# Performance work log

Measured on AMD Instinct MI355X. Metric: run time of the kernel, lower is better.

Reference implementation:

```python
import jax, jax.numpy as jnp
import numpy as np

_EPS = 1e-5

def _ln(x, g, b):
    m = jnp.mean(x, axis=-1, keepdims=True)
    v = jnp.var(x, axis=-1, keepdims=True)
    return (x - m) * jax.lax.rsqrt(v + _EPS) * g + b

def setup_inputs() -> dict:
    key = jax.random.key(0)
    ks = jax.random.split(key, 12)
    B, S, D = 8, 2048, 1024
    H = 2 * D          # hidden_dim = 2*n_embd
    A = H // 16        # adapt_dim = 128
    E = 8              # num_experts
    std = 1.0 / D ** 0.5
    astd = std * 0.01
    f = lambda k, shape, s: jax.random.normal(k, shape, dtype=jnp.float32) * s
    return {
        'x': f(ks[0], (B, S, D), 1.0),
        'expert_weights': f(ks[1], (B, S, E), 1.0),
        'w_up': f(ks[2], (H, D), std),
        'w_gate': f(ks[3], (H, D), std),
        'w_down': f(ks[4], (D, H), std),
        'w_pre': f(ks[5], (A, D), astd),
        'w_post': f(ks[6], (A, H), astd),
        'an_g': jnp.ones((A,), jnp.float32),
        'an_b': jnp.zeros((A,), jnp.float32),
        'w_aproj': f(ks[7], (H, A), astd),
        'w_exp': f(ks[8], (E, A, A), 0.01 / A ** 0.5),
        'eln_g': jnp.ones((E, A), jnp.float32),
        'eln_b': jnp.zeros((E, A), jnp.float32),
        'w_eproj': f(ks[9], (H, A), 0.01 / A ** 0.5),
        'w_out': f(ks[10], (D, H), 0.01 / A ** 0.5),
    }

def reference(x, expert_weights, w_up, w_gate, w_down, w_pre, w_post,
              an_g, an_b, w_aproj, w_exp, eln_g, eln_b, w_eproj, w_out):
    # ---- shared LLaDAExpert ----
    up = jnp.einsum('bsd,hd->bsh', x, w_up)
    gate = jnp.einsum('bsd,hd->bsh', x, w_gate)
    hidden = jax.nn.silu(gate) * up                      # [B,S,H]
    pre = jnp.einsum('bsd,ad->bsa', x, w_pre)            # pre_adapt(x), reused by experts
    adapt_in = _ln(pre, an_g, an_b)                      # [B,S,A]
    adapt_out = _ln(jnp.einsum('bsh,ah->bsa', hidden, w_post), an_g, an_b)
    aw = jax.nn.silu(jnp.clip(jnp.einsum('bsa,bta->bst', adapt_in, adapt_out), -5.0, 5.0))  # [B,S,S]
    adapt = jnp.einsum('bst,bta->bsa', aw, adapt_in)     # [B,S,A]
    hidden = hidden + 0.1 * jnp.einsum('bsa,ha->bsh', adapt, w_aproj)
    shared = jnp.einsum('bsh,dh->bsd', hidden, w_down)   # [B,S,D]
    combined = jnp.zeros_like(shared)
    E = w_exp.shape[0]
    for i in range(E):
        a = _ln(jnp.einsum('bsa,ca->bsc', pre, w_exp[i]), eln_g[i], eln_b[i])
        o = jnp.einsum('bsh,dh->bsd', jnp.einsum('bsc,hc->bsh', a, w_eproj), w_out)
        mask = expert_weights[:, :, i] > 0
        combined = jnp.where(mask[..., None], o, combined)
    return shared + 0.1 * combined
```

## Files before the change

kernel.cpp:

```cpp
#include <hip/hip_runtime.h>

#define TOK 16384
#define DD 1024
#define HH 2048
#define AA 128
#define EE 8
#define SS 2048
#define BB 8

typedef __attribute__((ext_vector_type(8))) short short8;
typedef __attribute__((ext_vector_type(4))) float floatx4;

__device__ __forceinline__ unsigned short f2b(float f) {
  unsigned u = __float_as_uint(f);
  u += 0x7fff + ((u >> 16) & 1);
  return (unsigned short)(u >> 16);
}
__device__ __forceinline__ float b2f(unsigned short h) {
  return __uint_as_float(((unsigned)h) << 16);
}

__device__ __forceinline__ void xcd_swizzle(int& bx, int& by) {
  const int nbx = gridDim.x, nby = gridDim.y;
  if ((nby & 7) == 0) {
    const int L = blockIdx.y * nbx + blockIdx.x;
    const int xcd = L & 7, idx = L >> 3;
    bx = idx % nbx;
    by = (xcd * (nby >> 3)) + idx / nbx;
  } else {
    bx = blockIdx.x; by = blockIdx.y;
  }
}


__device__ __forceinline__ void gload16(const short* g, short* l) {
  __builtin_amdgcn_global_load_lds((__attribute__((address_space(1))) void*)(void*)g,
                                   (__attribute__((address_space(3))) void*)l, 16, 0, 0);
}

__device__ __forceinline__ void stage_tile(const short* src, int ld, short* dst, int wave) {
#pragma unroll
  for (int i = 0; i < 4; ++i)
    gload16(src + (long)i*64*ld, dst + i*4096 + wave*512);
}

#define MFMA_BLK(MM0, NN0)                                                               \
  __builtin_amdgcn_s_setprio(1);                                                         \
  _Pragma("unroll")                                                                      \
  for (int m = 0; m < 4; ++m)                                                            \
    _Pragma("unroll")                                                                    \
    for (int n = 0; n < 2; ++n) {                                                        \
      acc[MM0+m][NN0+n] = __builtin_amdgcn_mfma_f32_16x16x32_bf16(af[MM0+m][0], bf[NN0+n][0], acc[MM0+m][NN0+n], 0, 0, 0); \
      acc[MM0+m][NN0+n] = __builtin_amdgcn_mfma_f32_16x16x32_bf16(af[MM0+m][1], bf[NN0+n][1], acc[MM0+m][NN0+n], 0, 0, 0); \
    }                                                                                    \
  __builtin_amdgcn_s_setprio(0);

__device__ __forceinline__ void ktile256(const char* Ab, const char* Bb,
                                         const char* An, const char* Bn,
                                         short* Ad, short* Bd,
                                         const short* sA, int slda,
                                         const short* sB, int sldb,
                                         bool st, bool rd, int wave,
                                         int aOff, int bOff, int slot0, int slot1,
                                         short8 (&af)[8][2], short8 (&bf)[4][2],
                                         floatx4 (*acc)[4])
{
#pragma unroll
  for (int n = 2; n < 4; ++n) {
    bf[n][0] = *(const short8*)(Bb + bOff + n*2048 + slot0);
    bf[n][1] = *(const short8*)(Bb + bOff + n*2048 + slot1);
  }
  MFMA_BLK(0, 0)
#pragma unroll
  for (int m = 4; m < 8; ++m) {
    af[m][0] = *(const short8*)(Ab + aOff + m*2048 + slot0);
    af[m][1] = *(const short8*)(Ab + aOff + m*2048 + slot1);
  }
  MFMA_BLK(0, 2)
  asm volatile("s_waitcnt lgkmcnt(0)" ::: "memory");
  __builtin_amdgcn_s_barrier();
  if (st) stage_tile(sB, sldb, Bd, wave);
  MFMA_BLK(4, 0)
  if (st) asm volatile("s_waitcnt vmcnt(4)" ::: "memory");
  else    asm volatile("s_waitcnt vmcnt(0)" ::: "memory");
  __builtin_amdgcn_s_barrier();
  if (rd) {
#pragma unroll
    for (int m = 0; m < 4; ++m) {
      af[m][0] = *(const short8*)(An + aOff + m*2048 + slot0);
      af[m][1] = *(const short8*)(An + aOff + m*2048 + slot1);
    }
#pragma unroll
    for (int n = 0; n < 2; ++n) {
      bf[n][0] = *(const short8*)(Bn + bOff + n*2048 + slot0);
      bf[n][1] = *(const short8*)(Bn + bOff + n*2048 + slot1);
    }
  }
  if (st) stage_tile(sA, slda, Ad, wave);
  MFMA_BLK(4, 2)
}

template<int EPI, bool SEG2>
__global__ __launch_bounds__(512, 2)
void gemm256(const unsigned short* __restrict__ Ag, int lda,
             const unsigned short* __restrict__ Bg, int ldb,
             void* __restrict__ Cg, int ldc,
             const unsigned short* __restrict__ Xg, int ldx,
             int K1,
             const unsigned short* __restrict__ A2g, int lda2,
             const unsigned short* __restrict__ B2g, int ldb2,
             int K2)
{
  __shared__ __align__(16) short As[2][256*64];
  __shared__ __align__(16) short Bs[2][256*64];
  int bx, by; xcd_swizzle(bx, by);
  const int tid = threadIdx.x;
  const int lane = tid & 63, wave = tid >> 6;
  const int q = lane >> 4, l15 = lane & 15;
  const int wm = wave >> 2, wn = wave & 3;

  const int arow = tid >> 3;
  const int kc8  = ((tid & 7) ^ (arow & 7)) * 8;

  const short* a1 = (const short*)Ag + (long)(by*256 + arow)*lda + kc8;
  const short* b1 = (const short*)Bg + (long)(bx*256 + arow)*ldb + kc8;
  const short* a2 = SEG2 ? (const short*)A2g + (long)(by*256 + arow)*lda2 + kc8 : (const short*)0;
  const short* b2 = SEG2 ? (const short*)B2g + (long)(bx*256 + arow)*ldb2 + kc8 : (const short*)0;
  const int nt1 = K1 >> 6, nt = SEG2 ? ((K1 + K2) >> 6) : (K1 >> 6);
  const int niter = nt >> 1;

  auto tA = [&](int T, const short*& p, int& ld) {
    if (!SEG2 || T < nt1) { p = a1 + T*64; ld = lda; } else { p = a2 + (T - nt1)*64; ld = lda2; }
  };
  auto tB = [&](int T, const short*& p, int& ld) {
    if (!SEG2 || T < nt1) { p = b1 + T*64; ld = ldb; } else { p = b2 + (T - nt1)*64; ld = ldb2; }
  };

  const int aOff  = (wm*128 + l15) * 128;
  const int bOff  = (wn*64  + l15) * 128;
  const int l7    = l15 & 7;
  const int slot0 = ((0*4 + q) ^ l7) * 16;
  const int slot1 = ((1*4 + q) ^ l7) * 16;

  floatx4 acc[8][4] = {};

  stage_tile(a1, lda, As[0], wave);
  stage_tile(b1, ldb, Bs[0], wave);
  {
    const short *pa, *pb; int la, lb;
    tA(1, pa, la); tB(1, pb, lb);
    stage_tile(pa, la, As[1], wave);
    stage_tile(pb, lb, Bs[1], wave);
  }
  asm volatile("s_waitcnt vmcnt(8)" ::: "memory");
  __builtin_amdgcn_s_barrier();

  short8 af[8][2], bf[4][2];
#pragma unroll
  for (int m = 0; m < 4; ++m) {
    af[m][0] = *(const short8*)((const char*)As[0] + aOff + m*2048 + slot0);
    af[m][1] = *(const short8*)((const char*)As[0] + aOff + m*2048 + slot1);
  }
#pragma unroll
  for (int n = 0; n < 2; ++n) {
    bf[n][0] = *(const short8*)((const char*)Bs[0] + bOff + n*2048 + slot0);
    bf[n][1] = *(const short8*)((const char*)Bs[0] + bOff + n*2048 + slot1);
  }

  for (int i = 0; i < niter; ++i) {
    const int t2 = 2*i + 2;
    const bool st = t2 < nt;
    const short *sa = a1, *sb = b1; int sla = lda, slb = ldb;
    if (st) { tA(t2, sa, sla); tB(t2, sb, slb); }
    ktile256((const char*)As[0], (const char*)Bs[0], (const char*)As[1], (const char*)Bs[1],
             As[0], Bs[0], sa, sla, sb, slb, st, true, wave,
             aOff, bOff, slot0, slot1, af, bf, acc);
    if (st) { tA(t2+1, sa, sla); tB(t2+1, sb, slb); }
    ktile256((const char*)As[1], (const char*)Bs[1], (const char*)As[0], (const char*)Bs[0],
             As[1], Bs[1], sa, sla, sb, slb, st, st, wave,
             aOff, bOff, slot0, slot1, af, bf, acc);
  }

#pragma unroll
  for (int m = 0; m < 8; ++m)
#pragma unroll
    for (int n = 0; n < 4; ++n)
#pragma unroll
      for (int r = 0; r < 4; ++r) {
        const int row = by*256 + wm*128 + m*16 + q*4 + r;
        const int col = bx*256 + wn*64  + n*16 + l15;
        const long ci = (long)row*ldc + col;
        float v = acc[m][n][r];
        if (EPI == 0) {
          ((float*)Cg)[ci] = v;
        } else if (EPI == 1) {
          v = v / (1.f + __expf(-v));
          ((unsigned short*)Cg)[ci] = f2b(v);
        } else if (EPI == 2) {
          float g = b2f(Xg[(long)row*ldx + col]);
          ((unsigned short*)Cg)[ci] = f2b(v * g);
        }
      }
}

__device__ __forceinline__ void kloop_pipe(const short* Ap, int lda, const short* Bp, int ldb,
                                           short* As, short* Bs, int K,
                                           int tid, int q, int l15, int l7, int wm, int wn,
                                           floatx4 (*acc)[4])
{
  short8 pa[4], pb[4];
#pragma unroll
  for (int i = 0; i < 4; ++i) {
    pa[i] = *(const short8*)(Ap + (long)i*32*lda);
    pb[i] = *(const short8*)(Bp + (long)i*32*ldb);
  }
  for (int kt = 0; kt < K; kt += 64) {
#pragma unroll
    for (int i = 0; i < 4; ++i) {
      *(short8*)((char*)As + i*4096 + tid*16) = pa[i];
      *(short8*)((char*)Bs + i*4096 + tid*16) = pb[i];
    }
    __syncthreads();
    if (kt + 64 < K) {
#pragma unroll
      for (int i = 0; i < 4; ++i) {
        pa[i] = *(const short8*)(Ap + (long)i*32*lda + kt + 64);
        pb[i] = *(const short8*)(Bp + (long)i*32*ldb + kt + 64);
      }
    }
#pragma unroll
    for (int s = 0; s < 2; ++s) {
      short8 af[4], bf[4];
      const int slotoff = ((s*4 + q) ^ l7) * 16;
#pragma unroll
      for (int i = 0; i < 4; ++i) {
        af[i] = *(const short8*)((const char*)As + (wm*64 + i*16 + l15)*128 + slotoff);
        bf[i] = *(const short8*)((const char*)Bs + (wn*64 + i*16 + l15)*128 + slotoff);
      }
#pragma unroll
      for (int i = 0; i < 4; ++i)
#pragma unroll
        for (int j = 0; j < 4; ++j)
          acc[i][j] = __builtin_amdgcn_mfma_f32_16x16x32_bf16(af[i], bf[j], acc[i][j], 0, 0, 0);
    }
    __syncthreads();
  }
}

__global__ void cast_f32_bf16(const float* __restrict__ in, unsigned short* __restrict__ out, long n4) {
  long i = (long)blockIdx.x * blockDim.x + threadIdx.x;
  const long stride = (long)gridDim.x * blockDim.x;
  for (; i < n4; i += stride) {
    float4 v = ((const float4*)in)[i];
    ushort4 o;
    o.x = f2b(v.x); o.y = f2b(v.y); o.z = f2b(v.z); o.w = f2b(v.w);
    ((ushort4*)out)[i] = o;
  }
}

__global__ void transpose_cast(const float* __restrict__ in, unsigned short* __restrict__ out,
                               int R, int C) {
  __shared__ float t[32][33];
  const int lx = threadIdx.x & 31, ly = threadIdx.x >> 5;
  const int r0 = blockIdx.y * 32, c0 = blockIdx.x * 32;
#pragma unroll
  for (int i = 0; i < 32; i += 8)
    t[ly + i][lx] = in[(long)(r0 + ly + i) * C + (c0 + lx)];
  __syncthreads();
#pragma unroll
  for (int i = 0; i < 32; i += 8)
    out[(long)(c0 + ly + i) * R + (r0 + lx)] = f2b(t[lx][ly + i]);
}

template<int EPI>
__global__ __launch_bounds__(256)
void gemm_bt(const unsigned short* __restrict__ Ag, long sAz, int lda,
             const unsigned short* __restrict__ Bg, long sBz, int ldb,
             void* __restrict__ Cg, long sCz, int ldc,
             const unsigned short* __restrict__ Xg, long sXz, int ldx,
             int K)
{
  __shared__ __align__(16) short As[128*64];
  __shared__ __align__(16) short Bs[128*64];
  int bx, by; xcd_swizzle(bx, by);
  const int tid  = threadIdx.x;
  const int lane = tid & 63, wave = tid >> 6;
  const int q = lane >> 4, l15 = lane & 15, l7 = lane & 7;
  const int wm = wave & 1, wn = wave >> 1;

  const int arow = tid >> 3;
  const int kc8  = ((tid & 7) ^ (arow & 7)) * 8;

  const short* Ap = (const short*)Ag + (long)blockIdx.z*sAz + (long)(by*128 + arow)*lda + kc8;
  const short* Bp = (const short*)Bg + (long)blockIdx.z*sBz + (long)(bx*128 + arow)*ldb + kc8;

  floatx4 acc[4][4] = {};
  kloop_pipe(Ap, lda, Bp, ldb, As, Bs, K, tid, q, l15, l7, wm, wn, acc);

  const long cz = (long)blockIdx.z * sCz;
  const long xz = (long)blockIdx.z * sXz;
#pragma unroll
  for (int i = 0; i < 4; ++i)
#pragma unroll
    for (int j = 0; j < 4; ++j)
#pragma unroll
      for (int r = 0; r < 4; ++r) {
        const int row = by*128 + wm*64 + i*16 + q*4 + r;
        const int col = bx*128 + wn*64 + j*16 + l15;
        const long ci = cz + (long)row*ldc + col;
        float v = acc[i][j][r];
        if (EPI == 0) {
          ((float*)Cg)[ci] = v;
        } else if (EPI == 1) {
          v = v / (1.f + __expf(-v));
          ((unsigned short*)Cg)[ci] = f2b(v);
        } else if (EPI == 2) {
          float g = b2f(Xg[xz + (long)row*ldx + col]);
          ((unsigned short*)Cg)[ci] = f2b(v * g);
        } else if (EPI == 3) {
          ((unsigned short*)Cg)[ci] = f2b(v);
        } else if (EPI == 4) {
          v = fminf(fmaxf(v, -5.f), 5.f);
          v = v / (1.f + __expf(-v));
          ((unsigned short*)Cg)[ci] = f2b(v);
        } else if (EPI == 6) {
          ((unsigned short*)Cg)[ci] = f2b(0.1f * v);
        }
      }
}

__global__ void ln_rows(const float* __restrict__ X, const float* __restrict__ g,
                        const float* __restrict__ b, unsigned short* __restrict__ lnout,
                        unsigned short* __restrict__ rawout, unsigned short* __restrict__ tout)
{
  const int lane = threadIdx.x & 63, wave = threadIdx.x >> 6;
  const long t = (long)blockIdx.x*4 + wave;
  const float* x = X + t*AA;
  float x0 = x[lane], x1 = x[lane + 64];
  float s = x0 + x1, s2 = x0*x0 + x1*x1;
#pragma unroll
  for (int m = 1; m < 64; m <<= 1) {
    s  += __shfl_xor(s, m, 64);
    s2 += __shfl_xor(s2, m, 64);
  }
  float mean = s * (1.f/AA);
  float inv  = rsqrtf(s2*(1.f/AA) - mean*mean + 1e-5f);
  float y0 = (x0 - mean)*inv*g[lane] + b[lane];
  float y1 = (x1 - mean)*inv*g[lane+64] + b[lane+64];
  lnout[t*AA + lane]      = f2b(y0);
  lnout[t*AA + lane + 64] = f2b(y1);
  if (rawout) { rawout[t*AA+lane] = f2b(x0); rawout[t*AA+lane+64] = f2b(x1); }
  if (tout) {
    const long bb = t >> 11, si = t & (SS-1);
    tout[bb*(long)AA*SS + (long)lane*SS + si]      = f2b(y0);
    tout[bb*(long)AA*SS + (long)(lane+64)*SS + si] = f2b(y1);
  }
}

__global__ void expert_select_ln(const float* __restrict__ ew, const unsigned short* __restrict__ eall,
                                 const float* __restrict__ eg, const float* __restrict__ ebias,
                                 unsigned short* __restrict__ Fc)
{
  const int lane = threadIdx.x & 63, wave = threadIdx.x >> 6;
  const long t = (long)blockIdx.x*4 + wave;
  const float* w = ew + t*EE;
  int ie = -1;
#pragma unroll
  for (int i = 0; i < EE; ++i) if (w[i] > 0.f) ie = i;
  unsigned short o0 = 0, o1 = 0;
  if (ie >= 0) {
    float x0 = b2f(eall[t*(EE*AA) + ie*AA + lane]);
    float x1 = b2f(eall[t*(EE*AA) + ie*AA + lane + 64]);
    float s = x0 + x1, s2 = x0*x0 + x1*x1;
#pragma unroll
    for (int m = 1; m < 64; m <<= 1) { s += __shfl_xor(s, m, 64); s2 += __shfl_xor(s2, m, 64); }
    float mean = s * (1.f/AA);
    float inv  = rsqrtf(s2*(1.f/AA) - mean*mean + 1e-5f);
    o0 = f2b((x0-mean)*inv*eg[ie*AA+lane]    + ebias[ie*AA+lane]);
    o1 = f2b((x1-mean)*inv*eg[ie*AA+lane+64] + ebias[ie*AA+lane+64]);
  }
  Fc[t*256 + lane]      = o0;
  Fc[t*256 + lane + 64] = o1;
}

extern "C" void kernel_launch(void* const* d_in, const int* in_sizes, int n_in,
                              void* d_out, int out_size, void* d_ws, size_t ws_size,
                              hipStream_t stream)
{
  const float* x       = (const float*)d_in[0];
  const float* ew      = (const float*)d_in[1];
  const float* w_up    = (const float*)d_in[2];
  const float* w_gate  = (const float*)d_in[3];
  const float* w_down  = (const float*)d_in[4];
  const float* w_pre   = (const float*)d_in[5];
  const float* w_post  = (const float*)d_in[6];
  const float* an_g    = (const float*)d_in[7];
  const float* an_b    = (const float*)d_in[8];
  const float* w_aproj = (const float*)d_in[9];
  const float* w_exp   = (const float*)d_in[10];
  const float* eln_g   = (const float*)d_in[11];
  const float* eln_b   = (const float*)d_in[12];
  const float* w_eproj = (const float*)d_in[13];
  const float* w_out   = (const float*)d_in[14];

  char* ws = (char*)d_ws;
  size_t off = 0;
  auto take = [&](size_t bytes) { char* p = ws + off; off += (bytes + 255) & ~(size_t)255; return p; };

  unsigned short* Sc    = (unsigned short*)take((size_t)BB*SS*SS*2);
  unsigned short* xb    = Sc;
  unsigned short* eall  = (unsigned short*)((char*)Sc + (size_t)TOK*DD*2);
  unsigned short* hid   = (unsigned short*)take((size_t)TOK*HH*2);
  float*          pre   = (float*)take((size_t)TOK*AA*4);
  float*          postA = (float*)take((size_t)TOK*AA*4);
  unsigned short* Fc    = (unsigned short*)take((size_t)TOK*256*2);
  unsigned short* ain   = (unsigned short*)take((size_t)TOK*AA*2);
  unsigned short* ainT  = (unsigned short*)take((size_t)TOK*AA*2);
  unsigned short* aout  = (unsigned short*)take((size_t)TOK*AA*2);
  unsigned short* preb  = (unsigned short*)take((size_t)TOK*AA*2);
  unsigned short* wgb   = (unsigned short*)take((size_t)HH*DD*2);
  unsigned short* wub   = (unsigned short*)take((size_t)HH*DD*2);
  unsigned short* wdb   = (unsigned short*)take((size_t)DD*HH*2);
  unsigned short* wpostb= (unsigned short*)take((size_t)AA*HH*2);
  unsigned short* wpreb = (unsigned short*)take((size_t)AA*DD*2);
  unsigned short* wexpb = (unsigned short*)take((size_t)EE*AA*AA*2);
  unsigned short* Wc    = (unsigned short*)take((size_t)DD*256*2);
  (void)ws_size; (void)in_sizes; (void)n_in; (void)out_size;

  unsigned short* woutb  = hid;
  unsigned short* btT    = hid + (size_t)DD*HH;
  unsigned short* eprojT = btT;
  unsigned short* aprojT = btT + (size_t)AA*HH;

  cast_f32_bf16<<<1024, 256, 0, stream>>>(x,      xb,     (long)TOK*DD/4);
  cast_f32_bf16<<<256,  256, 0, stream>>>(w_gate, wgb,    (long)HH*DD/4);
  cast_f32_bf16<<<256,  256, 0, stream>>>(w_up,   wub,    (long)HH*DD/4);
  cast_f32_bf16<<<256,  256, 0, stream>>>(w_down, wdb,    (long)DD*HH/4);
  cast_f32_bf16<<<256,  256, 0, stream>>>(w_out,  woutb,  (long)DD*HH/4);
  cast_f32_bf16<<<64,   256, 0, stream>>>(w_post, wpostb, (long)AA*HH/4);
  cast_f32_bf16<<<32,   256, 0, stream>>>(w_pre,  wpreb,  (long)AA*DD/4);
  cast_f32_bf16<<<32,   256, 0, stream>>>(w_exp,  wexpb,  (long)EE*AA*AA/4);

  transpose_cast<<<dim3(AA/32, HH/32), 256, 0, stream>>>(w_eproj, eprojT, HH, AA);
  transpose_cast<<<dim3(AA/32, HH/32), 256, 0, stream>>>(w_aproj, aprojT, HH, AA);

  gemm_bt<6><<<dim3(1, DD/128, 2), 256, 0, stream>>>(
      woutb, (long)(wdb - woutb), HH,
      eprojT, (long)AA*HH, HH,
      Wc, AA, 256, nullptr, 0, 0, HH);

  gemm256<1, false><<<dim3(HH/256, TOK/256), 512, 0, stream>>>(
      xb, DD, wgb, DD, hid, HH, nullptr, 0, DD, nullptr, 0, nullptr, 0, 0);
  gemm256<2, false><<<dim3(HH/256, TOK/256), 512, 0, stream>>>(
      xb, DD, wub, DD, hid, HH, hid, HH, DD, nullptr, 0, nullptr, 0, 0);

  gemm_bt<0><<<dim3(1, TOK/128, 1), 256, 0, stream>>>(xb,0,DD, wpreb,0,DD, pre,0,AA, nullptr,0,0, DD);
  ln_rows<<<TOK/4, 256, 0, stream>>>(pre, an_g, an_b, ain, preb, ainT);

  gemm_bt<3><<<dim3((EE*AA)/128, TOK/128, 1), 256, 0, stream>>>(preb,0,AA, wexpb,0,AA, eall,0,EE*AA, nullptr,0,0, AA);
  expert_select_ln<<<TOK/4, 256, 0, stream>>>(ew, eall, eln_g, eln_b, Fc);

  gemm_bt<0><<<dim3(1, TOK/128, 1), 256, 0, stream>>>(hid,0,HH, wpostb,0,HH, postA,0,AA, nullptr,0,0, HH);
  ln_rows<<<TOK/4, 256, 0, stream>>>(postA, an_g, an_b, aout, nullptr, nullptr);

  gemm_bt<4><<<dim3(SS/128, SS/128, BB), 256, 0, stream>>>(ain,(long)SS*AA,AA, aout,(long)SS*AA,AA,
                                                           Sc,(long)SS*SS,SS, nullptr,0,0, AA);
  gemm_bt<3><<<dim3(1, SS/128, BB), 256, 0, stream>>>(Sc,(long)SS*SS,SS, ainT,(long)AA*SS,SS,
                                                      Fc+AA,(long)SS*256,256, nullptr,0,0, SS);
  gemm256<0, true><<<dim3(DD/256, TOK/256), 512, 0, stream>>>(
      hid, HH, wdb, HH, (float*)d_out, DD, nullptr, 0, HH, Fc, 256, Wc, 256, 256);
}
```

Before: 610.7 us.

## Reschedule gemm256 into four barriered MFMA phases and split-K the narrow adapter GEMMs

The 256x256 GEMM main loop is rewritten into four phases per k-tile. Each phase is separated by barriers with explicit lgkmcnt/vmcnt waits, and the A and B tiles are staged at staggered times so global-to-LDS loads overlap more MFMA work. Separately, the two N=128 projection GEMMs (pre and post adapter), which launched only TOK/128 blocks, now split K in two via the batch dimension to double parallelism. The two partial sums are added inside ln_rows. This costs extra barriers per tile, twice the fp32 workspace for the partials, and an extra read of the second partial.

```diff
diff --git a/kernel.cpp b/kernel.cpp
--- a/kernel.cpp
+++ b/kernel.cpp
@@ -44,60 +44,76 @@
     gload16(src + (long)i*64*ld, dst + i*4096 + wave*512);
 }
 
-#define MFMA_BLK(MM0, NN0)                                                               \
+#define PHASE_MFMA(LG, M0, N0)                                                           \
+  __builtin_amdgcn_s_barrier();                                                          \
+  asm volatile("s_waitcnt lgkmcnt(" #LG ")" ::: "memory");                               \
+  __builtin_amdgcn_sched_barrier(0);                                                     \
   __builtin_amdgcn_s_setprio(1);                                                         \
   _Pragma("unroll")                                                                      \
-  for (int m = 0; m < 4; ++m)                                                            \
+  for (int kk = 0; kk < 2; ++kk)                                                         \
     _Pragma("unroll")                                                                    \
-    for (int n = 0; n < 2; ++n) {                                                        \
-      acc[MM0+m][NN0+n] = __builtin_amdgcn_mfma_f32_16x16x32_bf16(af[MM0+m][0], bf[NN0+n][0], acc[MM0+m][NN0+n], 0, 0, 0); \
-      acc[MM0+m][NN0+n] = __builtin_amdgcn_mfma_f32_16x16x32_bf16(af[MM0+m][1], bf[NN0+n][1], acc[MM0+m][NN0+n], 0, 0, 0); \
-    }                                                                                    \
-  __builtin_amdgcn_s_setprio(0);
-
-__device__ __forceinline__ void ktile256(const char* Ab, const char* Bb,
-                                         const char* An, const char* Bn,
-                                         short* Ad, short* Bd,
-                                         const short* sA, int slda,
-                                         const short* sB, int sldb,
-                                         bool st, bool rd, int wave,
-                                         int aOff, int bOff, int slot0, int slot1,
-                                         short8 (&af)[8][2], short8 (&bf)[4][2],
-                                         floatx4 (*acc)[4])
-{
+    for (int m = 0; m < 4; ++m)                                                          \
+      _Pragma("unroll")                                                                  \
+      for (int n = 0; n < 2; ++n)                                                        \
+        acc[M0+m][N0+n] = __builtin_amdgcn_mfma_f32_16x16x32_bf16(af[M0+m][kk], bf[N0+n][kk], acc[M0+m][N0+n], 0, 0, 0); \
+  __builtin_amdgcn_s_setprio(0);                                                         \
+  __builtin_amdgcn_s_barrier();
+
+__device__ __forceinline__ void ktile8(const char* cA, const char* cB,
+                                       const char* nB,
+                                       short* nAd, short* cBd,
+                                       const short* sA1, int lA1,
+                                       const short* sB2, int lB2,
+                                       bool stA, bool stB, bool rd, int wave,
+                                       int aOff, int bOff, int slot0, int slot1,
+                                       short8 (&af)[8][2], short8 (&bf)[4][2],
+                                       floatx4 (*acc)[4])
+{
+#pragma unroll
+  for (int m = 0; m < 4; ++m) {
+    af[m][0] = *(const short8*)(cA + aOff + m*2048 + slot0);
+    af[m][1] = *(const short8*)(cA + aOff + m*2048 + slot1);
+  }
+#pragma unroll
+  for (int m = 4; m < 8; ++m) {
+    af[m][0] = *(const short8*)(cA + aOff + m*2048 + slot0);
+    af[m][1] = *(const short8*)(cA + aOff + m*2048 + slot1);
+  }
+  if (stA) {
+    gload16(sA1 + 0L*64*lA1, nAd + 0*4096 + wave*512);
+    gload16(sA1 + 1L*64*lA1, nAd + 1*4096 + wave*512);
+  }
+  PHASE_MFMA(8, 0, 0)
 #pragma unroll
   for (int n = 2; n < 4; ++n) {
-    bf[n][0] = *(const short8*)(Bb + bOff + n*2048 + slot0);
-    bf[n][1] = *(const short8*)(Bb + bOff + n*2048 + slot1);
-  }
-  MFMA_BLK(0, 0)
-#pragma unroll
-  for (int m = 4; m < 8; ++m) {
-    af[m][0] = *(const short8*)(Ab + aOff + m*2048 + slot0);
-    af[m][1] = *(const short8*)(Ab + aOff + m*2048 + slot1);
-  }
-  MFMA_BLK(0, 2)
-  asm volatile("s_waitcnt lgkmcnt(0)" ::: "memory");
-  __builtin_amdgcn_s_barrier();
-  if (st) stage_tile(sB, sldb, Bd, wave);
-  MFMA_BLK(4, 0)
-  if (st) asm volatile("s_waitcnt vmcnt(4)" ::: "memory");
-  else    asm volatile("s_waitcnt vmcnt(0)" ::: "memory");
-  __builtin_amdgcn_s_barrier();
+    bf[n][0] = *(const short8*)(cB + bOff + n*2048 + slot0);
+    bf[n][1] = *(const short8*)(cB + bOff + n*2048 + slot1);
+  }
+  if (stA) {
+    gload16(sA1 + 2L*64*lA1, nAd + 2*4096 + wave*512);
+    gload16(sA1 + 3L*64*lA1, nAd + 3*4096 + wave*512);
+  }
+  asm volatile("s_waitcnt vmcnt(4)" ::: "memory");
+  PHASE_MFMA(4, 4, 0)
   if (rd) {
 #pragma unroll
-    for (int m = 0; m < 4; ++m) {
-      af[m][0] = *(const short8*)(An + aOff + m*2048 + slot0);
-      af[m][1] = *(const short8*)(An + aOff + m*2048 + slot1);
+    for (int n = 0; n < 2; ++n) {
+      bf[n][0] = *(const short8*)(nB + bOff + n*2048 + slot0);
+      bf[n][1] = *(const short8*)(nB + bOff + n*2048 + slot1);
     }
-#pragma unroll
-    for (int n = 0; n < 2; ++n) {
-      bf[n][0] = *(const short8*)(Bn + bOff + n*2048 + slot0);
-      bf[n][1] = *(const short8*)(Bn + bOff + n*2048 + slot1);
-    }
-  }
-  if (st) stage_tile(sA, slda, Ad, wave);
-  MFMA_BLK(4, 2)
+    PHASE_MFMA(4, 0, 2)
+  } else {
+    PHASE_MFMA(0, 0, 2)
+  }
+  if (stB) {
+#pragma unroll
+    for (int i = 0; i < 4; ++i)
+      gload16(sB2 + (long)i*64*lB2, cBd + i*4096 + wave*512);
+    asm volatile("s_waitcnt vmcnt(4)" ::: "memory");
+  } else {
+    asm volatile("s_waitcnt vmcnt(0)" ::: "memory");
+  }
+  PHASE_MFMA(4, 4, 2)
 }
 
 template<int EPI, bool SEG2>
@@ -111,8 +127,8 @@
              const unsigned short* __restrict__ B2g, int ldb2,
              int K2)
 {
-  __shared__ __align__(16) short As[2][256*64];
-  __shared__ __align__(16) short Bs[2][256*64];
+  __shared__ __align__(16) short As0[256*64], As1[256*64];
+  __shared__ __align__(16) short Bs0[256*64], Bs1[256*64];
   int bx, by; xcd_swizzle(bx, by);
   const int tid = threadIdx.x;
   const int lane = tid & 63, wave = tid >> 6;
@@ -127,7 +143,6 @@
   const short* a2 = SEG2 ? (const short*)A2g + (long)(by*256 + arow)*lda2 + kc8 : (const short*)0;
   const short* b2 = SEG2 ? (const short*)B2g + (long)(bx*256 + arow)*ldb2 + kc8 : (const short*)0;
   const int nt1 = K1 >> 6, nt = SEG2 ? ((K1 + K2) >> 6) : (K1 >> 6);
-  const int niter = nt >> 1;
 
   auto tA = [&](int T, const short*& p, int& ld) {
     if (!SEG2 || T < nt1) { p = a1 + T*64; ld = lda; } else { p = a2 + (T - nt1)*64; ld = lda2; }
@@ -143,42 +158,35 @@
   const int slot1 = ((1*4 + q) ^ l7) * 16;
 
   floatx4 acc[8][4] = {};
-
-  stage_tile(a1, lda, As[0], wave);
-  stage_tile(b1, ldb, Bs[0], wave);
+  short8 af[8][2], bf[4][2];
+
+  stage_tile(a1, lda, As0, wave);
+  stage_tile(b1, ldb, Bs0, wave);
   {
-    const short *pa, *pb; int la, lb;
-    tA(1, pa, la); tB(1, pb, lb);
-    stage_tile(pa, la, As[1], wave);
-    stage_tile(pb, lb, Bs[1], wave);
-  }
-  asm volatile("s_waitcnt vmcnt(8)" ::: "memory");
+    const short *pb; int lb;
+    tB(1, pb, lb);
+    stage_tile(pb, lb, Bs1, wave);
+  }
+  asm volatile("s_waitcnt vmcnt(4)" ::: "memory");
   __builtin_amdgcn_s_barrier();
-
-  short8 af[8][2], bf[4][2];
-#pragma unroll
-  for (int m = 0; m < 4; ++m) {
-    af[m][0] = *(const short8*)((const char*)As[0] + aOff + m*2048 + slot0);
-    af[m][1] = *(const short8*)((const char*)As[0] + aOff + m*2048 + slot1);
-  }
 #pragma unroll
   for (int n = 0; n < 2; ++n) {
-    bf[n][0] = *(const short8*)((const char*)Bs[0] + bOff + n*2048 + slot0);
-    bf[n][1] = *(const short8*)((const char*)Bs[0] + bOff + n*2048 + slot1);
-  }
-
-  for (int i = 0; i < niter; ++i) {
-    const int t2 = 2*i + 2;
-    const bool st = t2 < nt;
-    const short *sa = a1, *sb = b1; int sla = lda, slb = ldb;
-    if (st) { tA(t2, sa, sla); tB(t2, sb, slb); }
-    ktile256((const char*)As[0], (const char*)Bs[0], (const char*)As[1], (const char*)Bs[1],
-             As[0], Bs[0], sa, sla, sb, slb, st, true, wave,
-             aOff, bOff, slot0, slot1, af, bf, acc);
-    if (st) { tA(t2+1, sa, sla); tB(t2+1, sb, slb); }
-    ktile256((const char*)As[1], (const char*)Bs[1], (const char*)As[0], (const char*)Bs[0],
-             As[1], Bs[1], sa, sla, sb, slb, st, st, wave,
-             aOff, bOff, slot0, slot1, af, bf, acc);
+    bf[n][0] = *(const short8*)((const char*)Bs0 + bOff + n*2048 + slot0);
+    bf[n][1] = *(const short8*)((const char*)Bs0 + bOff + n*2048 + slot1);
+  }
+
+  for (int t = 0; t < nt; t += 2) {
+    const short *pa, *pb, *qa, *qb; int la, lb, qla, qlb;
+    const bool stA0 = (t+1) < nt, stB0 = (t+2) < nt;
+    tA(t+1, pa, la); tB(t+2, pb, lb);
+    ktile8((const char*)As0, (const char*)Bs0, (const char*)Bs1,
+           As1, Bs0, pa, la, pb, lb, stA0, stB0, stA0, wave,
+           aOff, bOff, slot0, slot1, af, bf, acc);
+    const bool stA1 = (t+2) < nt, stB1 = (t+3) < nt;
+    tA(t+2, qa, qla); tB(t+3, qb, qlb);
+    ktile8((const char*)As1, (const char*)Bs1, (const char*)Bs0,
+           As0, Bs1, qa, qla, qb, qlb, stA1, stB1, stA1, wave,
+           aOff, bOff, slot0, slot1, af, bf, acc);
   }
 
 #pragma unroll
@@ -329,14 +337,17 @@
       }
 }
 
-__global__ void ln_rows(const float* __restrict__ X, const float* __restrict__ g,
+__global__ void ln_rows(const float* __restrict__ X, const float* __restrict__ X2,
+                        const float* __restrict__ g,
                         const float* __restrict__ b, unsigned short* __restrict__ lnout,
                         unsigned short* __restrict__ rawout, unsigned short* __restrict__ tout)
 {
   const int lane = threadIdx.x & 63, wave = threadIdx.x >> 6;
   const long t = (long)blockIdx.x*4 + wave;
-  const float* x = X + t*AA;
-  float x0 = x[lane], x1 = x[lane + 64];
+  const float* x  = X  + t*AA;
+  const float* x2 = X2 + t*AA;
+  float x0 = x[lane]      + x2[lane];
+  float x1 = x[lane + 64] + x2[lane + 64];
   float s = x0 + x1, s2 = x0*x0 + x1*x1;
 #pragma unroll
   for (int m = 1; m < 64; m <<= 1) {
@@ -411,8 +422,8 @@
   unsigned short* xb    = Sc;
   unsigned short* eall  = (unsigned short*)((char*)Sc + (size_t)TOK*DD*2);
   unsigned short* hid   = (unsigned short*)take((size_t)TOK*HH*2);
-  float*          pre   = (float*)take((size_t)TOK*AA*4);
-  float*          postA = (float*)take((size_t)TOK*AA*4);
+  float*          pre   = (float*)take((size_t)TOK*AA*4*2);
+  float*          postA = (float*)take((size_t)TOK*AA*4*2);
   unsigned short* Fc    = (unsigned short*)take((size_t)TOK*256*2);
   unsigned short* ain   = (unsigned short*)take((size_t)TOK*AA*2);
   unsigned short* ainT  = (unsigned short*)take((size_t)TOK*AA*2);
@@ -454,14 +465,16 @@
   gemm256<2, false><<<dim3(HH/256, TOK/256), 512, 0, stream>>>(
       xb, DD, wub, DD, hid, HH, hid, HH, DD, nullptr, 0, nullptr, 0, 0);
 
-  gemm_bt<0><<<dim3(1, TOK/128, 1), 256, 0, stream>>>(xb,0,DD, wpreb,0,DD, pre,0,AA, nullptr,0,0, DD);
-  ln_rows<<<TOK/4, 256, 0, stream>>>(pre, an_g, an_b, ain, preb, ainT);
+  gemm_bt<0><<<dim3(1, TOK/128, 2), 256, 0, stream>>>(
+      xb, DD/2, DD, wpreb, DD/2, DD, pre, (long)TOK*AA, AA, nullptr, 0, 0, DD/2);
+  ln_rows<<<TOK/4, 256, 0, stream>>>(pre, pre + (size_t)TOK*AA, an_g, an_b, ain, preb, ainT);
 
   gemm_bt<3><<<dim3((EE*AA)/128, TOK/128, 1), 256, 0, stream>>>(preb,0,AA, wexpb,0,AA, eall,0,EE*AA, nullptr,0,0, AA);
   expert_select_ln<<<TOK/4, 256, 0, stream>>>(ew, eall, eln_g, eln_b, Fc);
 
-  gemm_bt<0><<<dim3(1, TOK/128, 1), 256, 0, stream>>>(hid,0,HH, wpostb,0,HH, postA,0,AA, nullptr,0,0, HH);
-  ln_rows<<<TOK/4, 256, 0, stream>>>(postA, an_g, an_b, aout, nullptr, nullptr);
+  gemm_bt<0><<<dim3(1, TOK/128, 2), 256, 0, stream>>>(
+      hid, HH/2, HH, wpostb, HH/2, HH, postA, (long)TOK*AA, AA, nullptr, 0, 0, HH/2);
+  ln_rows<<<TOK/4, 256, 0, stream>>>(postA, postA + (size_t)TOK*AA, an_g, an_b, aout, nullptr, nullptr);
 
   gemm_bt<4><<<dim3(SS/128, SS/128, BB), 256, 0, stream>>>(ain,(long)SS*AA,AA, aout,(long)SS*AA,AA,
                                                            Sc,(long)SS*SS,SS, nullptr,0,0, AA);
```

Result: slower. 1.130 ms (+85.1%).
